# Kernel optimization log

Measured on AMD Instinct MI355X. Metric: run time of the kernel, lower is better.

## Reference

```python
import jax, jax.numpy as jnp
import numpy as np

EMB = 128
NUM_RADIAL = 6
NUM_DENSE = 3
NUM_TARGETS = 12
N_EDGES = 640000
N_ATOMS = 20000


def setup_inputs() -> dict:
    key = jax.random.key(0)
    ks = jax.random.split(key, 12)
    inp = {
        "x": jax.random.normal(ks[0], (N_EDGES, EMB), dtype=jnp.float32),
        "rbf": jax.random.normal(ks[1], (N_EDGES, NUM_RADIAL), dtype=jnp.float32),
        "idnb_i": jax.random.randint(ks[2], (N_EDGES,), 0, N_ATOMS, dtype=jnp.int64),
        "n_atoms": N_ATOMS,
        # parameters
        "W_rbf": jax.random.normal(ks[3], (NUM_RADIAL, EMB), dtype=jnp.float32) * 0.1,  # no bias
        "dense_Ws": jax.random.normal(ks[4], (NUM_DENSE, EMB, EMB), dtype=jnp.float32) * (1.0 / np.sqrt(EMB)),
        "dense_bs": jax.random.normal(ks[5], (NUM_DENSE, EMB), dtype=jnp.float32) * 0.01,
        "W_final": jax.random.normal(ks[6], (EMB, NUM_TARGETS), dtype=jnp.float32) * (1.0 / np.sqrt(EMB)),  # no bias
    }
    return inp


def reference(x, rbf, idnb_i, n_atoms, W_rbf, dense_Ws, dense_bs, W_final):
    # gate: dense_rbf(rbf) * x, fused elementwise
    g = rbf @ W_rbf                      # [E, emb]
    xg = g * x                           # [E, emb]
    # scatter_add over edge -> atom indices
    h = jax.ops.segment_sum(xg, idnb_i, num_segments=n_atoms)  # [n_atoms, emb]
    # dense MLP head with swish activation
    for i in range(NUM_DENSE):
        h = jax.nn.silu(h @ dense_Ws[i] + dense_bs[i])
    return h @ W_final                   # [n_atoms, num_targets]
```

## Files before the change

kernel.cpp:

```cpp
#include <hip/hip_runtime.h>

#define EMB 128
#define NRAD 6
#define NT 12
#define NE 640000
#define NA 20000
#define SLOTS 128
#define HS_LD (EMB + 4)

__global__ __launch_bounds__(256) void zero_cnt(int* __restrict__ cnt) {
    int i = blockIdx.x * 256 + threadIdx.x;
    if (i < NA) cnt[i] = 0;
}

__global__ __launch_bounds__(256) void scatter_perm(const int* __restrict__ idx,
                                                    int* __restrict__ cnt,
                                                    int* __restrict__ perm) {
    int e = blockIdx.x * 256 + threadIdx.x;
    if (e < NE) {
        int a = idx[e];
        int pos = atomicAdd(&cnt[a], 1);
        if (pos < SLOTS) perm[(long long)a * SLOTS + pos] = e;
    }
}

__global__ __launch_bounds__(64) void gather_h(
    const float* __restrict__ x, const float* __restrict__ rbf,
    const float* __restrict__ Wrbf, const int* __restrict__ perm,
    const int* __restrict__ cnt, float* __restrict__ h)
{
    int a = blockIdx.x, t = threadIdx.x;
    float2 w[NRAD];
    #pragma unroll
    for (int i = 0; i < NRAD; ++i)
        w[i] = *reinterpret_cast<const float2*>(&Wrbf[i * EMB + 2 * t]);

    int n = cnt[a]; if (n > SLOTS) n = SLOTS;
    const int* prow = perm + (long long)a * SLOTS;

    float2 acc0 = {0.f, 0.f}, acc1 = {0.f, 0.f}, acc2 = {0.f, 0.f}, acc3 = {0.f, 0.f};
    float2 acc4 = {0.f, 0.f}, acc5 = {0.f, 0.f}, acc6 = {0.f, 0.f}, acc7 = {0.f, 0.f};

    auto body = [&](int j, float2& ac) {
        int edge = prow[j];
        const float* rp = rbf + (long long)edge * NRAD;
        float2 r01 = *reinterpret_cast<const float2*>(rp);
        float2 r23 = *reinterpret_cast<const float2*>(rp + 2);
        float2 r45 = *reinterpret_cast<const float2*>(rp + 4);
        float g0, g1;
        g0 = r01.x * w[0].x;            g1 = r01.x * w[0].y;
        g0 = fmaf(r01.y, w[1].x, g0);   g1 = fmaf(r01.y, w[1].y, g1);
        g0 = fmaf(r23.x, w[2].x, g0);   g1 = fmaf(r23.x, w[2].y, g1);
        g0 = fmaf(r23.y, w[3].x, g0);   g1 = fmaf(r23.y, w[3].y, g1);
        g0 = fmaf(r45.x, w[4].x, g0);   g1 = fmaf(r45.x, w[4].y, g1);
        g0 = fmaf(r45.y, w[5].x, g0);   g1 = fmaf(r45.y, w[5].y, g1);
        float2 xv = *reinterpret_cast<const float2*>(&x[(long long)edge * EMB + 2 * t]);
        ac.x = fmaf(g0, xv.x, ac.x);
        ac.y = fmaf(g1, xv.y, ac.y);
    };

    int j = 0;
    for (; j + 8 <= n; j += 8) {
        body(j + 0, acc0); body(j + 1, acc1); body(j + 2, acc2); body(j + 3, acc3);
        body(j + 4, acc4); body(j + 5, acc5); body(j + 6, acc6); body(j + 7, acc7);
    }
    for (; j < n; ++j) body(j, acc0);

    float2 r = {acc0.x + acc1.x + acc2.x + acc3.x + acc4.x + acc5.x + acc6.x + acc7.x,
                acc0.y + acc1.y + acc2.y + acc3.y + acc4.y + acc5.y + acc6.y + acc7.y};
    *reinterpret_cast<float2*>(&h[(long long)a * EMB + 2 * t]) = r;
}

__global__ __launch_bounds__(256) void mlp_head(
    const float* __restrict__ h, const float* __restrict__ Ws,
    const float* __restrict__ bs, const float* __restrict__ Wf,
    float* __restrict__ out)
{
    __shared__ float hs[32][HS_LD];
    __shared__ float wt[2][16 * EMB];

    const int t  = threadIdx.x;
    const int ab = blockIdx.x * 32;

    for (int i = t; i < 32 * 32; i += 256) {
        int row = i >> 5, c4 = (i & 31) << 2;
        *reinterpret_cast<float4*>(&hs[row][c4]) =
            *reinterpret_cast<const float4*>(&h[(long long)(ab + row) * EMB + c4]);
    }

    auto load_tile = [&](int g, int buf) {
        const float4* s4 = reinterpret_cast<const float4*>(Ws + (long long)g * 16 * EMB);
        float4* wdst = reinterpret_cast<float4*>(wt[buf]);
        wdst[t]       = s4[t];
        wdst[t + 256] = s4[t + 256];
    };
    load_tile(0, 0);

    const int jg = t & 31, j0 = jg * 4;
    const int ag = t >> 5, a0 = ag * 4;

    for (int l = 0; l < 3; ++l) {
        float4 bv = *reinterpret_cast<const float4*>(&bs[l * EMB + j0]);
        float acc[4][4];
        #pragma unroll
        for (int ai = 0; ai < 4; ++ai) {
            acc[ai][0] = bv.x; acc[ai][1] = bv.y; acc[ai][2] = bv.z; acc[ai][3] = bv.w;
        }

        for (int kt = 0; kt < 8; ++kt) {
            int g = l * 8 + kt;
            __syncthreads();
            if (g + 1 < 24) load_tile(g + 1, (g + 1) & 1);
            const float* wtc = wt[g & 1];
            #pragma unroll
            for (int q = 0; q < 4; ++q) {
                float4 w0 = *reinterpret_cast<const float4*>(&wtc[(q * 4 + 0) * EMB + j0]);
                float4 w1 = *reinterpret_cast<const float4*>(&wtc[(q * 4 + 1) * EMB + j0]);
                float4 w2 = *reinterpret_cast<const float4*>(&wtc[(q * 4 + 2) * EMB + j0]);
                float4 w3 = *reinterpret_cast<const float4*>(&wtc[(q * 4 + 3) * EMB + j0]);
                #pragma unroll
                for (int ai = 0; ai < 4; ++ai) {
                    float4 hv = *reinterpret_cast<const float4*>(&hs[a0 + ai][kt * 16 + q * 4]);
                    acc[ai][0] = fmaf(hv.x, w0.x, acc[ai][0]);
                    acc[ai][1] = fmaf(hv.x, w0.y, acc[ai][1]);
                    acc[ai][2] = fmaf(hv.x, w0.z, acc[ai][2]);
                    acc[ai][3] = fmaf(hv.x, w0.w, acc[ai][3]);
                    acc[ai][0] = fmaf(hv.y, w1.x, acc[ai][0]);
                    acc[ai][1] = fmaf(hv.y, w1.y, acc[ai][1]);
                    acc[ai][2] = fmaf(hv.y, w1.z, acc[ai][2]);
                    acc[ai][3] = fmaf(hv.y, w1.w, acc[ai][3]);
                    acc[ai][0] = fmaf(hv.z, w2.x, acc[ai][0]);
                    acc[ai][1] = fmaf(hv.z, w2.y, acc[ai][1]);
                    acc[ai][2] = fmaf(hv.z, w2.z, acc[ai][2]);
                    acc[ai][3] = fmaf(hv.z, w2.w, acc[ai][3]);
                    acc[ai][0] = fmaf(hv.w, w3.x, acc[ai][0]);
                    acc[ai][1] = fmaf(hv.w, w3.y, acc[ai][1]);
                    acc[ai][2] = fmaf(hv.w, w3.z, acc[ai][2]);
                    acc[ai][3] = fmaf(hv.w, w3.w, acc[ai][3]);
                }
            }
        }
        __syncthreads();
        #pragma unroll
        for (int ai = 0; ai < 4; ++ai) {
            #pragma unroll
            for (int ji = 0; ji < 4; ++ji) {
                float z = acc[ai][ji];
                acc[ai][ji] = z / (1.f + __expf(-z));
            }
            float4 v = make_float4(acc[ai][0], acc[ai][1], acc[ai][2], acc[ai][3]);
            *reinterpret_cast<float4*>(&hs[a0 + ai][j0]) = v;
        }
    }

    __syncthreads();
    for (int i = t; i < EMB * NT / 4; i += 256)
        reinterpret_cast<float4*>(wt[0])[i] = reinterpret_cast<const float4*>(Wf)[i];
    __syncthreads();

    for (int i = t; i < 32 * NT; i += 256) {
        int a = i / NT, jj = i - a * NT;
        float s = 0.f;
        #pragma unroll 4
        for (int k = 0; k < EMB; ++k) s = fmaf(hs[a][k], wt[0][k * NT + jj], s);
        out[(long long)(ab + a) * NT + jj] = s;
    }
}

extern "C" void kernel_launch(void* const* d_in, const int* in_sizes, int n_in,
                              void* d_out, int out_size, void* d_ws, size_t ws_size,
                              hipStream_t stream) {
    const float* x    = (const float*)d_in[0];
    const float* rbf  = (const float*)d_in[1];
    const int*   idx  = (const int*)d_in[2];
    const float* Wrbf = (const float*)d_in[4];
    const float* Ws   = (const float*)d_in[5];
    const float* bsp  = (const float*)d_in[6];
    const float* Wf   = (const float*)d_in[7];
    float* out = (float*)d_out;

    char* ws = (char*)d_ws;
    float* h    = (float*)ws;
    int*   cnt  = (int*)(ws + (size_t)NA * EMB * 4);
    int*   perm = cnt + 20032;

    zero_cnt    <<<(NA + 255) / 256, 256, 0, stream>>>(cnt);
    scatter_perm<<<(NE + 255) / 256, 256, 0, stream>>>(idx, cnt, perm);
    gather_h    <<<NA, 64, 0, stream>>>(x, rbf, Wrbf, perm, cnt, h);
    mlp_head    <<<NA / 32, 256, 0, stream>>>(h, Ws, bsp, Wf, out);
}
```

Baseline: 160.1 us.

## Fuse the edge gather into the MLP head kernel and memset the counts

The per-atom gather-and-gate kernel is merged into the MLP head kernel. Each 512-thread block now has its 8 waves each accumulate 4 atoms directly into shared memory, so the intermediate h array is never written to or read back from global memory. The MLP tiling is adjusted to 2 rows per thread to match the larger block. The zero-count kernel is replaced by hipMemsetAsync. The trade-off is far fewer independent waves for the latency-bound gather, since each wave walks 4 atoms in series, which may cut memory-level parallelism.

```diff
diff --git a/kernel.cpp b/kernel.cpp
--- a/kernel.cpp
+++ b/kernel.cpp
@@ -7,11 +7,6 @@
 #define NA 20000
 #define SLOTS 128
 #define HS_LD (EMB + 4)
-
-__global__ __launch_bounds__(256) void zero_cnt(int* __restrict__ cnt) {
-    int i = blockIdx.x * 256 + threadIdx.x;
-    if (i < NA) cnt[i] = 0;
-}
 
 __global__ __launch_bounds__(256) void scatter_perm(const int* __restrict__ idx,
                                                     int* __restrict__ cnt,
@@ -24,86 +19,80 @@
     }
 }
 
-__global__ __launch_bounds__(64) void gather_h(
+__global__ __launch_bounds__(512) void fused_gather_mlp(
     const float* __restrict__ x, const float* __restrict__ rbf,
     const float* __restrict__ Wrbf, const int* __restrict__ perm,
-    const int* __restrict__ cnt, float* __restrict__ h)
-{
-    int a = blockIdx.x, t = threadIdx.x;
-    float2 w[NRAD];
-    #pragma unroll
-    for (int i = 0; i < NRAD; ++i)
-        w[i] = *reinterpret_cast<const float2*>(&Wrbf[i * EMB + 2 * t]);
-
-    int n = cnt[a]; if (n > SLOTS) n = SLOTS;
-    const int* prow = perm + (long long)a * SLOTS;
-
-    float2 acc0 = {0.f, 0.f}, acc1 = {0.f, 0.f}, acc2 = {0.f, 0.f}, acc3 = {0.f, 0.f};
-    float2 acc4 = {0.f, 0.f}, acc5 = {0.f, 0.f}, acc6 = {0.f, 0.f}, acc7 = {0.f, 0.f};
-
-    auto body = [&](int j, float2& ac) {
-        int edge = prow[j];
-        const float* rp = rbf + (long long)edge * NRAD;
-        float2 r01 = *reinterpret_cast<const float2*>(rp);
-        float2 r23 = *reinterpret_cast<const float2*>(rp + 2);
-        float2 r45 = *reinterpret_cast<const float2*>(rp + 4);
-        float g0, g1;
-        g0 = r01.x * w[0].x;            g1 = r01.x * w[0].y;
-        g0 = fmaf(r01.y, w[1].x, g0);   g1 = fmaf(r01.y, w[1].y, g1);
-        g0 = fmaf(r23.x, w[2].x, g0);   g1 = fmaf(r23.x, w[2].y, g1);
-        g0 = fmaf(r23.y, w[3].x, g0);   g1 = fmaf(r23.y, w[3].y, g1);
-        g0 = fmaf(r45.x, w[4].x, g0);   g1 = fmaf(r45.x, w[4].y, g1);
-        g0 = fmaf(r45.y, w[5].x, g0);   g1 = fmaf(r45.y, w[5].y, g1);
-        float2 xv = *reinterpret_cast<const float2*>(&x[(long long)edge * EMB + 2 * t]);
-        ac.x = fmaf(g0, xv.x, ac.x);
-        ac.y = fmaf(g1, xv.y, ac.y);
-    };
-
-    int j = 0;
-    for (; j + 8 <= n; j += 8) {
-        body(j + 0, acc0); body(j + 1, acc1); body(j + 2, acc2); body(j + 3, acc3);
-        body(j + 4, acc4); body(j + 5, acc5); body(j + 6, acc6); body(j + 7, acc7);
-    }
-    for (; j < n; ++j) body(j, acc0);
-
-    float2 r = {acc0.x + acc1.x + acc2.x + acc3.x + acc4.x + acc5.x + acc6.x + acc7.x,
-                acc0.y + acc1.y + acc2.y + acc3.y + acc4.y + acc5.y + acc6.y + acc7.y};
-    *reinterpret_cast<float2*>(&h[(long long)a * EMB + 2 * t]) = r;
-}
-
-__global__ __launch_bounds__(256) void mlp_head(
-    const float* __restrict__ h, const float* __restrict__ Ws,
+    const int* __restrict__ cnt, const float* __restrict__ Ws,
     const float* __restrict__ bs, const float* __restrict__ Wf,
     float* __restrict__ out)
 {
     __shared__ float hs[32][HS_LD];
     __shared__ float wt[2][16 * EMB];
 
-    const int t  = threadIdx.x;
-    const int ab = blockIdx.x * 32;
+    const int t    = threadIdx.x;
+    const int wid  = t >> 6;
+    const int lane = t & 63;
+    const int ab   = blockIdx.x * 32;
 
-    for (int i = t; i < 32 * 32; i += 256) {
-        int row = i >> 5, c4 = (i & 31) << 2;
-        *reinterpret_cast<float4*>(&hs[row][c4]) =
-            *reinterpret_cast<const float4*>(&h[(long long)(ab + row) * EMB + c4]);
+    {
+        float2 w[NRAD];
+        #pragma unroll
+        for (int i = 0; i < NRAD; ++i)
+            w[i] = *reinterpret_cast<const float2*>(&Wrbf[i * EMB + 2 * lane]);
+
+        for (int ii = 0; ii < 4; ++ii) {
+            int row = wid * 4 + ii;
+            int a   = __builtin_amdgcn_readfirstlane(ab + row);
+            int n   = cnt[a]; if (n > SLOTS) n = SLOTS;
+            const int* prow = perm + (long long)a * SLOTS;
+
+            float2 acc0 = {0.f,0.f}, acc1 = {0.f,0.f}, acc2 = {0.f,0.f}, acc3 = {0.f,0.f};
+            float2 acc4 = {0.f,0.f}, acc5 = {0.f,0.f}, acc6 = {0.f,0.f}, acc7 = {0.f,0.f};
+
+            auto body = [&](int j, float2& ac) {
+                int edge = prow[j];
+                const float* rp = rbf + (long long)edge * NRAD;
+                float2 r01 = *reinterpret_cast<const float2*>(rp);
+                float2 r23 = *reinterpret_cast<const float2*>(rp + 2);
+                float2 r45 = *reinterpret_cast<const float2*>(rp + 4);
+                float g0, g1;
+                g0 = r01.x * w[0].x;            g1 = r01.x * w[0].y;
+                g0 = fmaf(r01.y, w[1].x, g0);   g1 = fmaf(r01.y, w[1].y, g1);
+                g0 = fmaf(r23.x, w[2].x, g0);   g1 = fmaf(r23.x, w[2].y, g1);
+                g0 = fmaf(r23.y, w[3].x, g0);   g1 = fmaf(r23.y, w[3].y, g1);
+                g0 = fmaf(r45.x, w[4].x, g0);   g1 = fmaf(r45.x, w[4].y, g1);
+                g0 = fmaf(r45.y, w[5].x, g0);   g1 = fmaf(r45.y, w[5].y, g1);
+                float2 xv = *reinterpret_cast<const float2*>(&x[(long long)edge * EMB + 2 * lane]);
+                ac.x = fmaf(g0, xv.x, ac.x);
+                ac.y = fmaf(g1, xv.y, ac.y);
+            };
+
+            int j = 0;
+            for (; j + 8 <= n; j += 8) {
+                body(j + 0, acc0); body(j + 1, acc1); body(j + 2, acc2); body(j + 3, acc3);
+                body(j + 4, acc4); body(j + 5, acc5); body(j + 6, acc6); body(j + 7, acc7);
+            }
+            for (; j < n; ++j) body(j, acc0);
+
+            hs[row][2 * lane]     = acc0.x + acc1.x + acc2.x + acc3.x + acc4.x + acc5.x + acc6.x + acc7.x;
+            hs[row][2 * lane + 1] = acc0.y + acc1.y + acc2.y + acc3.y + acc4.y + acc5.y + acc6.y + acc7.y;
+        }
     }
 
     auto load_tile = [&](int g, int buf) {
         const float4* s4 = reinterpret_cast<const float4*>(Ws + (long long)g * 16 * EMB);
-        float4* wdst = reinterpret_cast<float4*>(wt[buf]);
-        wdst[t]       = s4[t];
-        wdst[t + 256] = s4[t + 256];
+        reinterpret_cast<float4*>(wt[buf])[t] = s4[t];
     };
     load_tile(0, 0);
 
     const int jg = t & 31, j0 = jg * 4;
-    const int ag = t >> 5, a0 = ag * 4;
+    const int ag = t >> 5, a0 = ag * 2;
 
     for (int l = 0; l < 3; ++l) {
         float4 bv = *reinterpret_cast<const float4*>(&bs[l * EMB + j0]);
-        float acc[4][4];
+        float acc[2][4];
         #pragma unroll
-        for (int ai = 0; ai < 4; ++ai) {
+        for (int ai = 0; ai < 2; ++ai) {
             acc[ai][0] = bv.x; acc[ai][1] = bv.y; acc[ai][2] = bv.z; acc[ai][3] = bv.w;
         }
 
@@ -119,7 +108,7 @@
                 float4 w2 = *reinterpret_cast<const float4*>(&wtc[(q * 4 + 2) * EMB + j0]);
                 float4 w3 = *reinterpret_cast<const float4*>(&wtc[(q * 4 + 3) * EMB + j0]);
                 #pragma unroll
-                for (int ai = 0; ai < 4; ++ai) {
+                for (int ai = 0; ai < 2; ++ai) {
                     float4 hv = *reinterpret_cast<const float4*>(&hs[a0 + ai][kt * 16 + q * 4]);
                     acc[ai][0] = fmaf(hv.x, w0.x, acc[ai][0]);
                     acc[ai][1] = fmaf(hv.x, w0.y, acc[ai][1]);
@@ -142,7 +131,7 @@
         }
         __syncthreads();
         #pragma unroll
-        for (int ai = 0; ai < 4; ++ai) {
+        for (int ai = 0; ai < 2; ++ai) {
             #pragma unroll
             for (int ji = 0; ji < 4; ++ji) {
                 float z = acc[ai][ji];
@@ -154,12 +143,12 @@
     }
 
     __syncthreads();
-    for (int i = t; i < EMB * NT / 4; i += 256)
+    for (int i = t; i < EMB * NT / 4; i += 512)
         reinterpret_cast<float4*>(wt[0])[i] = reinterpret_cast<const float4*>(Wf)[i];
     __syncthreads();
 
-    for (int i = t; i < 32 * NT; i += 256) {
-        int a = i / NT, jj = i - a * NT;
+    if (t < 32 * NT) {
+        int a = t / NT, jj = t - a * NT;
         float s = 0.f;
         #pragma unroll 4
         for (int k = 0; k < EMB; ++k) s = fmaf(hs[a][k], wt[0][k * NT + jj], s);
@@ -180,12 +169,11 @@
     float* out = (float*)d_out;
 
     char* ws = (char*)d_ws;
-    float* h    = (float*)ws;
-    int*   cnt  = (int*)(ws + (size_t)NA * EMB * 4);
-    int*   perm = cnt + 20032;
+    int* cnt  = (int*)ws;
+    int* perm = cnt + 20032;
 
-    zero_cnt    <<<(NA + 255) / 256, 256, 0, stream>>>(cnt);
-    scatter_perm<<<(NE + 255) / 256, 256, 0, stream>>>(idx, cnt, perm);
-    gather_h    <<<NA, 64, 0, stream>>>(x, rbf, Wrbf, perm, cnt, h);
-    mlp_head    <<<NA / 32, 256, 0, stream>>>(h, Ws, bsp, Wf, out);
+    hipMemsetAsync(cnt, 0, (size_t)NA * sizeof(int), stream);
+    scatter_perm   <<<(NE + 255) / 256, 256, 0, stream>>>(idx, cnt, perm);
+    fused_gather_mlp<<<NA / 32, 512, 0, stream>>>(x, rbf, Wrbf, perm, cnt,
+                                                  Ws, bsp, Wf, out);
 }
```

Measured after the change: 150.7 us. 5.9% less time.
